# Kernel optimization log

Hardware: AMD Instinct MI355X
Metric: run time of the kernel (lower is better)

The kernel has to match this reference:

```python
import jax, jax.numpy as jnp
import numpy as np

B, S, D_IN, D_OUT, CAP = 4, 2048, 4096, 4096, 1024


def setup_inputs() -> dict:
    key = jax.random.key(0)
    k1, k2, k3, k4, k5 = jax.random.split(key, 5)
    x = jax.random.normal(k1, (B, S, D_IN), dtype=jnp.float32)
    # lattice-quantized weights (static buffer) and per-row scale
    weight_lattices = jax.random.normal(k2, (D_OUT, D_IN), dtype=jnp.float32)
    weight_scales = jax.random.uniform(k3, (D_OUT, 1), dtype=jnp.float32)
    # associative LatticeMemory: keys over input dim, values over output dim
    mem_keys = jax.random.normal(k4, (CAP, D_IN), dtype=jnp.float32)
    mem_values = jax.random.normal(k5, (CAP, D_OUT), dtype=jnp.float32)
    return {"x": x, "weight_lattices": weight_lattices,
            "weight_scales": weight_scales,
            "mem_keys": mem_keys, "mem_values": mem_values}


def reference(x, weight_lattices, weight_scales, mem_keys, mem_values):
    # dequantize: elementwise scale of the lattice codes -> full fp32 weight
    w_dequant = weight_lattices * weight_scales            # [O, I]
    # main GEMM: out = x @ w_dequant.T
    out = jnp.einsum('bsi,oi->bso', x, w_dequant)          # [B, S, O]
    # associative memory retrieval on the first flattened token
    q = x.reshape(-1, x.shape[-1])[0]                      # [I]
    attn = jax.nn.softmax(mem_keys @ q)                    # [CAP]
    memory_out = attn @ mem_values                         # [O]
    return out + 0.01 * memory_out
```

## Files before the change

### kernel.cpp

```cpp
#include <hip/hip_runtime.h>
#include <hip/hip_bf16.h>
#include <stdint.h>

#define D_IN   4096
#define D_OUT  4096
#define MROWS  8192
#define CAPN   1024
#define NT     64

typedef __bf16 bf16x8 __attribute__((ext_vector_type(8)));
typedef float f32x4 __attribute__((ext_vector_type(4)));

__device__ static inline void async_copy16(const void* g, void* l) {
  __builtin_amdgcn_global_load_lds((__attribute__((address_space(1))) void*)g,
                                   (__attribute__((address_space(3))) void*)l,
                                   16, 0, 0);
}

__global__ __launch_bounds__(256) void cvt_x_kernel(const float* __restrict__ x,
                                                    __hip_bfloat16* __restrict__ xb) {
  size_t i = ((size_t)blockIdx.x * 256 + threadIdx.x) * 8;
  float4 f0 = *(const float4*)(x + i);
  float4 f1 = *(const float4*)(x + i + 4);
  union { __hip_bfloat16 h[8]; uint4 u; } o;
  o.h[0] = __float2bfloat16(f0.x); o.h[1] = __float2bfloat16(f0.y);
  o.h[2] = __float2bfloat16(f0.z); o.h[3] = __float2bfloat16(f0.w);
  o.h[4] = __float2bfloat16(f1.x); o.h[5] = __float2bfloat16(f1.y);
  o.h[6] = __float2bfloat16(f1.z); o.h[7] = __float2bfloat16(f1.w);
  *(uint4*)(xb + i) = o.u;
}

__global__ __launch_bounds__(256) void cvt_w_kernel(const float* __restrict__ wl,
                                                    const float* __restrict__ wscale,
                                                    __hip_bfloat16* __restrict__ wb) {
  size_t i = ((size_t)blockIdx.x * 256 + threadIdx.x) * 8;
  int row = (int)(i >> 12);
  float s = wscale[row];
  float4 f0 = *(const float4*)(wl + i);
  float4 f1 = *(const float4*)(wl + i + 4);
  union { __hip_bfloat16 h[8]; uint4 u; } o;
  o.h[0] = __float2bfloat16(f0.x * s); o.h[1] = __float2bfloat16(f0.y * s);
  o.h[2] = __float2bfloat16(f0.z * s); o.h[3] = __float2bfloat16(f0.w * s);
  o.h[4] = __float2bfloat16(f1.x * s); o.h[5] = __float2bfloat16(f1.y * s);
  o.h[6] = __float2bfloat16(f1.z * s); o.h[7] = __float2bfloat16(f1.w * s);
  *(uint4*)(wb + i) = o.u;
}

__global__ __launch_bounds__(256) void mem_logits_kernel(const float* __restrict__ keys,
                                                         const float* __restrict__ q,
                                                         float* __restrict__ logits) {
  int c = blockIdx.x;
  const float* k = keys + (size_t)c * D_IN;
  float p = 0.f;
  for (int i = threadIdx.x; i < D_IN; i += 256) p += k[i] * q[i];
  for (int off = 32; off; off >>= 1) p += __shfl_down(p, off);
  __shared__ float r[4];
  if ((threadIdx.x & 63) == 0) r[threadIdx.x >> 6] = p;
  __syncthreads();
  if (threadIdx.x == 0) logits[c] = r[0] + r[1] + r[2] + r[3];
}

__global__ __launch_bounds__(256) void mem_attn_out_kernel(const float* __restrict__ logits,
                                                           const float* __restrict__ vals,
                                                           float* __restrict__ memo) {
  int tid = threadIdx.x;
  __shared__ float sa[1024];
  __shared__ float wm[4], ws[4];
  __shared__ float part[4][64];
  float4 lv = ((const float4*)logits)[tid];
  float m = fmaxf(fmaxf(lv.x, lv.y), fmaxf(lv.z, lv.w));
  for (int off = 32; off; off >>= 1) m = fmaxf(m, __shfl_down(m, off));
  if ((tid & 63) == 0) wm[tid >> 6] = m;
  __syncthreads();
  m = fmaxf(fmaxf(wm[0], wm[1]), fmaxf(wm[2], wm[3]));
  float e0 = __expf(lv.x - m), e1 = __expf(lv.y - m);
  float e2 = __expf(lv.z - m), e3 = __expf(lv.w - m);
  float s = e0 + e1 + e2 + e3;
  for (int off = 32; off; off >>= 1) s += __shfl_down(s, off);
  if ((tid & 63) == 0) ws[tid >> 6] = s;
  __syncthreads();
  float inv = 1.f / (ws[0] + ws[1] + ws[2] + ws[3]);
  sa[tid * 4 + 0] = e0 * inv; sa[tid * 4 + 1] = e1 * inv;
  sa[tid * 4 + 2] = e2 * inv; sa[tid * 4 + 3] = e3 * inv;
  __syncthreads();
  int g = tid >> 6, lane = tid & 63;
  int o = blockIdx.x * 64 + lane;
  float acc = 0.f;
  const float* vp = vals + (size_t)(g * 256) * D_OUT + o;
#pragma unroll 8
  for (int c = 0; c < 256; ++c) acc += sa[g * 256 + c] * vp[(size_t)c * D_OUT];
  part[g][lane] = acc;
  __syncthreads();
  if (tid < 64) memo[o] = part[0][lane] + part[1][lane] + part[2][lane] + part[3][lane];
}

__global__ __launch_bounds__(512, 2) void gemm_8ph_kernel(const __hip_bfloat16* __restrict__ A,
                                                          const __hip_bfloat16* __restrict__ Bm,
                                                          const float* __restrict__ memo,
                                                          float* __restrict__ C) {
  __shared__ bf16x8 LA[2][32][64];
  __shared__ bf16x8 LB[2][32][64];
  const int tid = threadIdx.x;
  const int l = tid & 63;
  const int w = tid >> 6;
  const int wr = w >> 2;
  const int wc = w & 3;
  const int w2 = w * 2;

  const int bid = blockIdx.x;
  const int swz = (bid & 7) * 64 + (bid >> 3);
  const int m_blk = (swz >> 4) * 256;
  const int n_blk = (swz & 15) * 256;

  const int lm = l & 15;
  const int lk = (l >> 4) * 8;

  const __hip_bfloat16* baseA0 = A  + (size_t)(m_blk + (0 * 8 + w) * 16 + lm) * D_IN + lk;
  const __hip_bfloat16* baseA1 = A  + (size_t)(m_blk + (1 * 8 + w) * 16 + lm) * D_IN + lk;
  const __hip_bfloat16* baseB0 = Bm + (size_t)(n_blk + (0 * 8 + w) * 16 + lm) * D_IN + lk;
  const __hip_bfloat16* baseB1 = Bm + (size_t)(n_blk + (1 * 8 + w) * 16 + lm) * D_IN + lk;

#define STAGE_A(h, T, sb) do {                                                   \
    async_copy16(baseA##h + (size_t)(T) * 64,      &LA[sb][(h) * 16 + w2][0]);   \
    async_copy16(baseA##h + (size_t)(T) * 64 + 32, &LA[sb][(h) * 16 + w2 + 1][0]); \
  } while (0)
#define STAGE_B(h, T, sb) do {                                                   \
    async_copy16(baseB##h + (size_t)(T) * 64,      &LB[sb][(h) * 16 + w2][0]);   \
    async_copy16(baseB##h + (size_t)(T) * 64 + 32, &LB[sb][(h) * 16 + w2 + 1][0]); \
  } while (0)

  f32x4 acc[8][4] = {};
  bf16x8 a[4][2], b[4][2];

#define BAR_MFMA(JH, IH)                                                         \
  do {                                                                           \
    __builtin_amdgcn_s_barrier();                                                \
    asm volatile("s_waitcnt lgkmcnt(0)" ::: "memory");                           \
    __builtin_amdgcn_sched_barrier(0);                                           \
    __builtin_amdgcn_s_setprio(1);                                               \
    _Pragma("unroll") for (int jj = 0; jj < 4; ++jj)                             \
    _Pragma("unroll") for (int i2 = 0; i2 < 2; ++i2)                             \
    _Pragma("unroll") for (int kk = 0; kk < 2; ++kk)                             \
      acc[(JH) * 4 + jj][(IH) * 2 + i2] = __builtin_amdgcn_mfma_f32_16x16x32_bf16( \
          a[jj][kk], b[(IH) * 2 + i2][kk], acc[(JH) * 4 + jj][(IH) * 2 + i2], 0, 0, 0); \
    __builtin_amdgcn_s_setprio(0);                                               \
    __builtin_amdgcn_sched_barrier(0);                                           \
    __builtin_amdgcn_s_barrier();                                                \
  } while (0)

#define TILE4(t, bb, DOS1, DOS2, VMSTMT)                                         \
  do {                                                                           \
                                                                        \
    _Pragma("unroll") for (int j = 0; j < 4; ++j) {                              \
      a[j][0] = LA[bb][(2 * j + wr) * 2 + 0][l];                                 \
      a[j][1] = LA[bb][(2 * j + wr) * 2 + 1][l];                                 \
    }                                                                            \
    _Pragma("unroll") for (int ii = 0; ii < 2; ++ii) {                           \
      b[ii][0] = LB[bb][(4 * ii + wc) * 2 + 0][l];                               \
      b[ii][1] = LB[bb][(4 * ii + wc) * 2 + 1][l];                               \
    }                                                                            \
    if (DOS1) { STAGE_A(1, (t) + 1, (bb) ^ 1); }                                 \
    BAR_MFMA(0, 0);                                                              \
                                                                        \
    _Pragma("unroll") for (int ii = 2; ii < 4; ++ii) {                           \
      b[ii][0] = LB[bb][(4 * ii + wc) * 2 + 0][l];                               \
      b[ii][1] = LB[bb][(4 * ii + wc) * 2 + 1][l];                               \
    }                                                                            \
    if (DOS2) { STAGE_A(0, (t) + 2, bb); }                                       \
    BAR_MFMA(0, 1);                                                              \
                                                                        \
    _Pragma("unroll") for (int j = 0; j < 4; ++j) {                              \
      a[j][0] = LA[bb][(2 * j + 8 + wr) * 2 + 0][l];                             \
      a[j][1] = LA[bb][(2 * j + 8 + wr) * 2 + 1][l];                             \
    }                                                                            \
    if (DOS2) { STAGE_B(0, (t) + 2, bb); }                                       \
    BAR_MFMA(1, 0);                                                              \
                                                                        \
    if (DOS2) { STAGE_B(1, (t) + 2, bb); }                                       \
    VMSTMT;                                                                      \
    BAR_MFMA(1, 1);                                                              \
  } while (0)

#define VM6 asm volatile("s_waitcnt vmcnt(6)" ::: "memory")
#define VM0 asm volatile("s_waitcnt vmcnt(0)" ::: "memory")
#define VMN ((void)0)

  STAGE_A(0, 0, 0); STAGE_B(0, 0, 0); STAGE_B(1, 0, 0); STAGE_A(1, 0, 0);
  STAGE_A(0, 1, 1); STAGE_B(0, 1, 1); STAGE_B(1, 1, 1);
  asm volatile("s_waitcnt vmcnt(6)" ::: "memory");
  __builtin_amdgcn_s_barrier();

#pragma unroll 1
  for (int t = 0; t < NT - 2; t += 2) {
    TILE4(t, 0, 1, 1, VM6);
    TILE4(t + 1, 1, 1, 1, VM6);
  }
  TILE4(NT - 2, 0, 1, 0, VM0);
  TILE4(NT - 1, 1, 0, 0, VMN);

  const int col_l = l & 15;
  const int row_l = (l >> 4) * 4;
#pragma unroll
  for (int ii = 0; ii < 4; ++ii) {
    int col = n_blk + (4 * ii + wc) * 16 + col_l;
    float mo = 0.01f * memo[col];
#pragma unroll
    for (int j = 0; j < 8; ++j) {
      int row = m_blk + (2 * j + wr) * 16 + row_l;
      float* cp = C + (size_t)row * D_OUT + col;
#pragma unroll
      for (int r = 0; r < 4; ++r) cp[(size_t)r * D_OUT] = acc[j][ii][r] + mo;
    }
  }
}

extern "C" void kernel_launch(void* const* d_in, const int* in_sizes, int n_in,
                              void* d_out, int out_size, void* d_ws, size_t ws_size,
                              hipStream_t stream) {
  const float* x   = (const float*)d_in[0];
  const float* wl  = (const float*)d_in[1];
  const float* wsc = (const float*)d_in[2];
  const float* mk  = (const float*)d_in[3];
  const float* mv  = (const float*)d_in[4];
  float* out = (float*)d_out;

  char* wsb = (char*)d_ws;
  __hip_bfloat16* xb = (__hip_bfloat16*)wsb;
  __hip_bfloat16* wb = (__hip_bfloat16*)(wsb + (size_t)MROWS * D_IN * 2);
  float* logits = (float*)(wsb + (size_t)MROWS * D_IN * 2 + (size_t)D_OUT * D_IN * 2);
  float* memo = logits + CAPN;

  cvt_x_kernel<<<dim3((MROWS * D_IN) / 2048), dim3(256), 0, stream>>>(x, xb);
  cvt_w_kernel<<<dim3((D_OUT * D_IN) / 2048), dim3(256), 0, stream>>>(wl, wsc, wb);

  mem_logits_kernel<<<dim3(CAPN), dim3(256), 0, stream>>>(mk, x, logits);
  mem_attn_out_kernel<<<dim3(D_OUT / 64), dim3(256), 0, stream>>>(logits, mv, memo);

  gemm_8ph_kernel<<<dim3((MROWS / 256) * (D_OUT / 256)), dim3(512), 0, stream>>>(xb, wb, memo, out);
}
```

Before: 659.1 us.

## Merge prep kernels into one launch and prefetch next B fragments inside GEMM

The x and weight bf16 conversions and the memory-logits kernel are merged into a single launch that splits work by block index, removing two launch gaps and the tail serialisation between them. In the GEMM, the first B-fragment LDS reads of the next tile are moved into the final MFMA phase of the current tile, issued right after the barrier. The explicit lgkmcnt(0) waits and sched_barriers are removed, and the MFMA loop order is changed to iterate k outermost. Dropping the explicit waits hands LDS-read synchronisation to the compiler. This risks a different schedule, or hazards if the compiler places waits poorly.

```diff
diff --git a/kernel.cpp b/kernel.cpp
--- a/kernel.cpp
+++ b/kernel.cpp
@@ -17,47 +17,47 @@
                                    16, 0, 0);
 }
 
-__global__ __launch_bounds__(256) void cvt_x_kernel(const float* __restrict__ x,
-                                                    __hip_bfloat16* __restrict__ xb) {
-  size_t i = ((size_t)blockIdx.x * 256 + threadIdx.x) * 8;
-  float4 f0 = *(const float4*)(x + i);
-  float4 f1 = *(const float4*)(x + i + 4);
-  union { __hip_bfloat16 h[8]; uint4 u; } o;
-  o.h[0] = __float2bfloat16(f0.x); o.h[1] = __float2bfloat16(f0.y);
-  o.h[2] = __float2bfloat16(f0.z); o.h[3] = __float2bfloat16(f0.w);
-  o.h[4] = __float2bfloat16(f1.x); o.h[5] = __float2bfloat16(f1.y);
-  o.h[6] = __float2bfloat16(f1.z); o.h[7] = __float2bfloat16(f1.w);
-  *(uint4*)(xb + i) = o.u;
-}
-
-__global__ __launch_bounds__(256) void cvt_w_kernel(const float* __restrict__ wl,
-                                                    const float* __restrict__ wscale,
-                                                    __hip_bfloat16* __restrict__ wb) {
-  size_t i = ((size_t)blockIdx.x * 256 + threadIdx.x) * 8;
-  int row = (int)(i >> 12);
-  float s = wscale[row];
-  float4 f0 = *(const float4*)(wl + i);
-  float4 f1 = *(const float4*)(wl + i + 4);
-  union { __hip_bfloat16 h[8]; uint4 u; } o;
-  o.h[0] = __float2bfloat16(f0.x * s); o.h[1] = __float2bfloat16(f0.y * s);
-  o.h[2] = __float2bfloat16(f0.z * s); o.h[3] = __float2bfloat16(f0.w * s);
-  o.h[4] = __float2bfloat16(f1.x * s); o.h[5] = __float2bfloat16(f1.y * s);
-  o.h[6] = __float2bfloat16(f1.z * s); o.h[7] = __float2bfloat16(f1.w * s);
-  *(uint4*)(wb + i) = o.u;
-}
-
-__global__ __launch_bounds__(256) void mem_logits_kernel(const float* __restrict__ keys,
-                                                         const float* __restrict__ q,
-                                                         float* __restrict__ logits) {
-  int c = blockIdx.x;
-  const float* k = keys + (size_t)c * D_IN;
-  float p = 0.f;
-  for (int i = threadIdx.x; i < D_IN; i += 256) p += k[i] * q[i];
-  for (int off = 32; off; off >>= 1) p += __shfl_down(p, off);
+__global__ __launch_bounds__(256) void prep_kernel(const float* __restrict__ x,
+                                                   __hip_bfloat16* __restrict__ xb,
+                                                   const float* __restrict__ wl,
+                                                   const float* __restrict__ wscale,
+                                                   __hip_bfloat16* __restrict__ wb,
+                                                   const float* __restrict__ keys,
+                                                   float* __restrict__ logits) {
   __shared__ float r[4];
-  if ((threadIdx.x & 63) == 0) r[threadIdx.x >> 6] = p;
-  __syncthreads();
-  if (threadIdx.x == 0) logits[c] = r[0] + r[1] + r[2] + r[3];
+  int bx = blockIdx.x;
+  if (bx < 16384) {
+    size_t i = ((size_t)bx * 256 + threadIdx.x) * 8;
+    float4 f0 = *(const float4*)(x + i);
+    float4 f1 = *(const float4*)(x + i + 4);
+    union { __hip_bfloat16 h[8]; uint4 u; } o;
+    o.h[0] = __float2bfloat16(f0.x); o.h[1] = __float2bfloat16(f0.y);
+    o.h[2] = __float2bfloat16(f0.z); o.h[3] = __float2bfloat16(f0.w);
+    o.h[4] = __float2bfloat16(f1.x); o.h[5] = __float2bfloat16(f1.y);
+    o.h[6] = __float2bfloat16(f1.z); o.h[7] = __float2bfloat16(f1.w);
+    *(uint4*)(xb + i) = o.u;
+  } else if (bx < 16384 + 8192) {
+    size_t i = ((size_t)(bx - 16384) * 256 + threadIdx.x) * 8;
+    int row = (int)(i >> 12);
+    float s = wscale[row];
+    float4 f0 = *(const float4*)(wl + i);
+    float4 f1 = *(const float4*)(wl + i + 4);
+    union { __hip_bfloat16 h[8]; uint4 u; } o;
+    o.h[0] = __float2bfloat16(f0.x * s); o.h[1] = __float2bfloat16(f0.y * s);
+    o.h[2] = __float2bfloat16(f0.z * s); o.h[3] = __float2bfloat16(f0.w * s);
+    o.h[4] = __float2bfloat16(f1.x * s); o.h[5] = __float2bfloat16(f1.y * s);
+    o.h[6] = __float2bfloat16(f1.z * s); o.h[7] = __float2bfloat16(f1.w * s);
+    *(uint4*)(wb + i) = o.u;
+  } else {
+    int c = bx - (16384 + 8192);
+    const float* k = keys + (size_t)c * D_IN;
+    float p = 0.f;
+    for (int i = threadIdx.x; i < D_IN; i += 256) p += k[i] * x[i];
+    for (int off = 32; off; off >>= 1) p += __shfl_down(p, off);
+    if ((threadIdx.x & 63) == 0) r[threadIdx.x >> 6] = p;
+    __syncthreads();
+    if (threadIdx.x == 0) logits[c] = r[0] + r[1] + r[2] + r[3];
+  }
 }
 
 __global__ __launch_bounds__(256) void mem_attn_out_kernel(const float* __restrict__ logits,
@@ -132,53 +132,56 @@
   f32x4 acc[8][4] = {};
   bf16x8 a[4][2], b[4][2];
 
-#define BAR_MFMA(JH, IH)                                                         \
+#define RD_BNEXT(sb) do {                                                        \
+    _Pragma("unroll") for (int ii = 0; ii < 2; ++ii) {                           \
+      b[ii][0] = LB[sb][(4 * ii + wc) * 2 + 0][l];                               \
+      b[ii][1] = LB[sb][(4 * ii + wc) * 2 + 1][l];                               \
+    } } while (0)
+
+#define BAR_MFMA(JH, IH, PRE)                                                    \
   do {                                                                           \
     __builtin_amdgcn_s_barrier();                                                \
-    asm volatile("s_waitcnt lgkmcnt(0)" ::: "memory");                           \
-    __builtin_amdgcn_sched_barrier(0);                                           \
+    PRE;                                                                         \
     __builtin_amdgcn_s_setprio(1);                                               \
+    _Pragma("unroll") for (int kk = 0; kk < 2; ++kk)                             \
     _Pragma("unroll") for (int jj = 0; jj < 4; ++jj)                             \
     _Pragma("unroll") for (int i2 = 0; i2 < 2; ++i2)                             \
-    _Pragma("unroll") for (int kk = 0; kk < 2; ++kk)                             \
       acc[(JH) * 4 + jj][(IH) * 2 + i2] = __builtin_amdgcn_mfma_f32_16x16x32_bf16( \
           a[jj][kk], b[(IH) * 2 + i2][kk], acc[(JH) * 4 + jj][(IH) * 2 + i2], 0, 0, 0); \
     __builtin_amdgcn_s_setprio(0);                                               \
-    __builtin_amdgcn_sched_barrier(0);                                           \
     __builtin_amdgcn_s_barrier();                                                \
   } while (0)
 
-#define TILE4(t, bb, DOS1, DOS2, VMSTMT)                                         \
+#define NOPRE ((void)0)
+
+#define TILE4(t, bb, DOS1, DOS2, DON, VMSTMT)                                    \
   do {                                                                           \
-                                                                        \
+                           \
     _Pragma("unroll") for (int j = 0; j < 4; ++j) {                              \
       a[j][0] = LA[bb][(2 * j + wr) * 2 + 0][l];                                 \
       a[j][1] = LA[bb][(2 * j + wr) * 2 + 1][l];                                 \
     }                                                                            \
-    _Pragma("unroll") for (int ii = 0; ii < 2; ++ii) {                           \
-      b[ii][0] = LB[bb][(4 * ii + wc) * 2 + 0][l];                               \
-      b[ii][1] = LB[bb][(4 * ii + wc) * 2 + 1][l];                               \
-    }                                                                            \
     if (DOS1) { STAGE_A(1, (t) + 1, (bb) ^ 1); }                                 \
-    BAR_MFMA(0, 0);                                                              \
-                                                                        \
+    BAR_MFMA(0, 0, NOPRE);                                                       \
+                                                 \
     _Pragma("unroll") for (int ii = 2; ii < 4; ++ii) {                           \
       b[ii][0] = LB[bb][(4 * ii + wc) * 2 + 0][l];                               \
       b[ii][1] = LB[bb][(4 * ii + wc) * 2 + 1][l];                               \
     }                                                                            \
     if (DOS2) { STAGE_A(0, (t) + 2, bb); }                                       \
-    BAR_MFMA(0, 1);                                                              \
-                                                                        \
+    BAR_MFMA(0, 1, NOPRE);                                                       \
+                                                       \
     _Pragma("unroll") for (int j = 0; j < 4; ++j) {                              \
       a[j][0] = LA[bb][(2 * j + 8 + wr) * 2 + 0][l];                             \
       a[j][1] = LA[bb][(2 * j + 8 + wr) * 2 + 1][l];                             \
     }                                                                            \
     if (DOS2) { STAGE_B(0, (t) + 2, bb); }                                       \
-    BAR_MFMA(1, 0);                                                              \
-                                                                        \
+    BAR_MFMA(1, 0, NOPRE);                                                       \
+        \
     if (DOS2) { STAGE_B(1, (t) + 2, bb); }                                       \
     VMSTMT;                                                                      \
-    BAR_MFMA(1, 1);                                                              \
+    if (DON) { BAR_MFMA(1, 1, RD_BNEXT((bb) ^ 1)); }                             \
+    else     { BAR_MFMA(1, 1, NOPRE); }                                          \
   } while (0)
 
 #define VM6 asm volatile("s_waitcnt vmcnt(6)" ::: "memory")
@@ -189,14 +192,15 @@
   STAGE_A(0, 1, 1); STAGE_B(0, 1, 1); STAGE_B(1, 1, 1);
   asm volatile("s_waitcnt vmcnt(6)" ::: "memory");
   __builtin_amdgcn_s_barrier();
+  RD_BNEXT(0);
 
 #pragma unroll 1
   for (int t = 0; t < NT - 2; t += 2) {
-    TILE4(t, 0, 1, 1, VM6);
-    TILE4(t + 1, 1, 1, 1, VM6);
+    TILE4(t, 0, 1, 1, 1, VM6);
+    TILE4(t + 1, 1, 1, 1, 1, VM6);
   }
-  TILE4(NT - 2, 0, 1, 0, VM0);
-  TILE4(NT - 1, 1, 0, 0, VMN);
+  TILE4(NT - 2, 0, 1, 0, 1, VM0);
+  TILE4(NT - 1, 1, 0, 0, 0, VMN);
 
   const int col_l = l & 15;
   const int row_l = (l >> 4) * 4;
@@ -230,10 +234,8 @@
   float* logits = (float*)(wsb + (size_t)MROWS * D_IN * 2 + (size_t)D_OUT * D_IN * 2);
   float* memo = logits + CAPN;
 
-  cvt_x_kernel<<<dim3((MROWS * D_IN) / 2048), dim3(256), 0, stream>>>(x, xb);
-  cvt_w_kernel<<<dim3((D_OUT * D_IN) / 2048), dim3(256), 0, stream>>>(wl, wsc, wb);
-
-  mem_logits_kernel<<<dim3(CAPN), dim3(256), 0, stream>>>(mk, x, logits);
+  prep_kernel<<<dim3(16384 + 8192 + 1024), dim3(256), 0, stream>>>(x, xb, wl, wsc, wb, mk, logits);
+
   mem_attn_out_kernel<<<dim3(D_OUT / 64), dim3(256), 0, stream>>>(logits, mv, memo);
 
   gemm_8ph_kernel<<<dim3((MROWS / 256) * (D_OUT / 256)), dim3(512), 0, stream>>>(xb, wb, memo, out);
```

New measurement: 693.6 us. +5.2%, slower.
